# Optimization experiments

Measured on AMD Instinct MI355X. Metric: run time of the kernel, lower is better.

The kernel has to match this reference:

```python
import jax, jax.numpy as jnp
import numpy as np

B, T, C, H = 4, 2048, 1024, 64  # batch, seq, embedding_size, head_size

def setup_inputs() -> dict:
    key = jax.random.key(0)
    k0, k1, k2, k3 = jax.random.split(key, 4)
    scale = 0.02
    return {
        "x":  jax.random.normal(k0, (B, T, C), dtype=jnp.float32),
        "Wq": jax.random.normal(k1, (H, C), dtype=jnp.float32) * scale,
        "Wk": jax.random.normal(k2, (H, C), dtype=jnp.float32) * scale,
        "Wv": jax.random.normal(k3, (H, C), dtype=jnp.float32) * scale,
    }

def reference(x, Wq, Wk, Wv):
    # Linear(bias=False): y = x @ W^T
    q = jnp.einsum('btc,hc->bth', x, Wq)
    k = jnp.einsum('btc,hc->bth', x, Wk)
    v = jnp.einsum('btc,hc->bth', x, Wv)
    # NOTE: original scales by embedding_size C**-0.5, not head_size
    wei = jnp.einsum('bth,bsh->bts', q, k) * (x.shape[-1] ** -0.5)
    t = x.shape[1]
    causal_mask = jnp.tril(jnp.ones((t, t), dtype=bool))  # [T, T]
    wei = jnp.where(causal_mask, wei, -jnp.inf)
    wei = jax.nn.softmax(wei, axis=-1)
    # dropout = 0.0 -> identity (eval mode)
    out = jnp.einsum('bts,bsh->bth', wei, v)
    return out
```

## Files before the change

### kernel.cpp

```cpp
#include <hip/hip_runtime.h>
#include <hip/hip_bf16.h>

typedef unsigned short u16;
typedef __attribute__((ext_vector_type(8))) __bf16 bf16x8;
typedef __attribute__((ext_vector_type(4))) float f32x4;

#define B_ 4
#define T_ 2048
#define C_ 1024
#define H_ 64
#define NSEG 8

__device__ __forceinline__ u16 f2bf(float f) {
    union { __hip_bfloat16 h; u16 u; } cv;
    cv.h = __float2bfloat16(f);
    return cv.u;
}

__device__ __forceinline__ float bf2f(unsigned v) {
    union { unsigned u; float f; } c; c.u = v << 16; return c.f;
}

__device__ __forceinline__ bf16x8 cvt8r(float4 f0, float4 f1) {
    union { u16 h[8]; bf16x8 v; } ua;
    ua.h[0] = f2bf(f0.x); ua.h[1] = f2bf(f0.y);
    ua.h[2] = f2bf(f0.z); ua.h[3] = f2bf(f0.w);
    ua.h[4] = f2bf(f1.x); ua.h[5] = f2bf(f1.y);
    ua.h[6] = f2bf(f1.z); ua.h[7] = f2bf(f1.w);
    return ua.v;
}

__device__ __forceinline__ void gll16(const void* g, void* l) {
    __builtin_amdgcn_global_load_lds(
        (const __attribute__((address_space(1))) void*)g,
        (__attribute__((address_space(3))) void*)l, 16, 0, 0);
}

__global__ __launch_bounds__(256) void wpack(
    const float* __restrict__ wq, const float* __restrict__ wk,
    const float* __restrict__ wv, u16* __restrict__ wP)
{
    int u    = blockIdx.x * 256 + threadIdx.x;
    int ln   = u & 63;
    int frag = u >> 6;
    int ksg  = frag & 31;
    int j16  = frag >> 5;
    int n    = j16 * 16 + (ln & 15);
    int kb   = ksg * 32 + (ln >> 4) * 8;
    const float* src = (n < 64) ? (wq + (size_t)n * C_)
                     : (n < 128) ? (wk + (size_t)(n - 64) * C_)
                                 : (wv + (size_t)(n - 128) * C_);
    float4 f0 = *(const float4*)(src + kb);
    float4 f1 = *(const float4*)(src + kb + 4);
    *(bf16x8*)(wP + (size_t)u * 8) = cvt8r(f0, f1);
}

__global__ __launch_bounds__(512) void qkv(
    const float* __restrict__ x, const u16* __restrict__ wP,
    u16* __restrict__ qP, u16* __restrict__ kP, u16* __restrict__ vP)
{
    __shared__ __align__(16) char smem[32768];

    const int tid = threadIdx.x;
    const int ln  = tid & 63;
    const int w   = tid >> 6;
    const int m0  = blockIdx.x * 32;

    const int lr = ln & 15;
    const int g  = ln >> 4;
    const int ms = w >> 2;
    const int nh = w & 3;

    f32x4 acc[3] = {};

    const int xrow = w * 4 + (ln >> 4);
    const int xc   = (ln & 15) ^ (xrow & 7);

#define STAGE(BUF, KC)                                                     \
    gll16(x + (size_t)(m0 + xrow) * C_ + (KC) * 64 + xc * 4,               \
          smem + (BUF) * 8192 + w * 1024)

    STAGE(0, 0);
    __syncthreads();

    const int ra  = ms * 16 + lr;
    const int rsw = ra & 7;
    const u16* wbase = wP + (size_t)(nh * 3) * 32 * 64 * 8;

    for (int kc = 0; kc < 16; ++kc) {
        const int buf = kc & 1;
        if (kc < 15) STAGE(buf ^ 1, kc + 1);

        const char* rb = smem + buf * 8192;

        bf16x8 a[2];
        #pragma unroll
        for (int ks = 0; ks < 2; ++ks) {
            int c0 = ks * 8 + g * 2;
            float4 fa = *(const float4*)(rb + ra * 256 + ((c0       ^ rsw) << 4));
            float4 fb = *(const float4*)(rb + ra * 256 + (((c0 + 1) ^ rsw) << 4));
            a[ks] = cvt8r(fa, fb);
        }

        #pragma unroll
        for (int j = 0; j < 3; ++j) {
            #pragma unroll
            for (int ks = 0; ks < 2; ++ks) {
                size_t fragofs = ((size_t)(j * 32 + kc * 2 + ks) * 64 + ln) * 8;
                bf16x8 b = *(const bf16x8*)(wbase + fragofs);
                acc[j] = __builtin_amdgcn_mfma_f32_16x16x32_bf16(a[ks], b, acc[j], 0, 0, 0);
            }
        }

        __syncthreads();
    }
#undef STAGE

    float* tile = (float*)smem;
    #pragma unroll
    for (int j = 0; j < 3; ++j)
        #pragma unroll
        for (int i = 0; i < 4; ++i)
            tile[(ms * 16 + g * 4 + i) * 201 + nh * 48 + j * 16 + lr] = acc[j][i];
    __syncthreads();

    for (int uu = tid; uu < 768; uu += 512) {
        const int ln2 = uu & 63;
        const int lr2 = ln2 & 15;
        const int g2  = ln2 >> 4;
        if (uu < 512) {
            const int isK = uu >> 8;
            const int rem = uu & 255;
            const int u   = rem >> 7;
            const int ks  = (rem >> 6) & 1;
            const float* src = tile + (u * 16 + lr2) * 201 + isK * 64 + ks * 32 + g2 * 8;
            float4 f0 = *(const float4*)src;
            float4 f1 = *(const float4*)(src + 4);
            bf16x8 val = cvt8r(f0, f1);
            u16* dst = (isK ? kP : qP)
                     + ((size_t)(((m0 >> 4) + u) * 2 + ks) * 64 + ln2) * 8;
            *(bf16x8*)dst = val;
        } else {
            const int rem = uu - 512;
            const int jf  = rem >> 6;
            union { u16 h[8]; bf16x8 v; } ua;
            #pragma unroll
            for (int e = 0; e < 8; ++e)
                ua.h[e] = f2bf(tile[(g2 * 8 + e) * 201 + 128 + jf * 16 + lr2]);
            u16* dst = vP + ((size_t)((m0 >> 5) * 4 + jf) * 64 + ln2) * 8;
            *(bf16x8*)dst = ua.v;
        }
    }
}

__global__ __launch_bounds__(64) void attn_part(
    const u16* __restrict__ qP, const u16* __restrict__ kP,
    const u16* __restrict__ vP, u16* __restrict__ opart,
    float* __restrict__ ml)
{
    __shared__ u16 ps[16 * 72];

    const int lane = threadIdx.x;
    const int bid  = blockIdx.x;
    const int seg  = bid & (NSEG - 1);
    const int tix  = bid >> 3;
    const int b    = tix & 3;
    const int qt   = 127 - (tix >> 2);
    const int q0   = qt * 16;

    const int lr = lane & 15;
    const int g  = lane >> 4;
    const int lk = g * 8;

    const int nch = (qt >> 2) + 1;
    const int L   = (nch + NSEG - 1) >> 3;
    const int c0  = seg * L;
    const int c1  = min(nch, c0 + L);

    if (c0 >= c1) {
        if (lr == 0)
            #pragma unroll
            for (int i = 0; i < 4; ++i) {
                ml[(size_t)bid * 32 + (g * 4 + i) * 2]     = -1e30f;
                ml[(size_t)bid * 32 + (g * 4 + i) * 2 + 1] = 0.f;
            }
        return;
    }

    bf16x8 aq[2];
    #pragma unroll
    for (int ks = 0; ks < 2; ++ks)
        aq[ks] = *(const bf16x8*)(qP + ((size_t)((b * 128 + qt) * 2 + ks) * 64 + lane) * 8);

    f32x4 oacc[4] = {};
    float mrow[4], lrow[4];
    #pragma unroll
    for (int i = 0; i < 4; ++i) { mrow[i] = -1e30f; lrow[i] = 0.f; }

    for (int jc = c0; jc < c1; ++jc) {
        const int kv0 = jc << 6;

        bf16x8 bk[8];
        #pragma unroll
        for (int jf = 0; jf < 4; ++jf)
            #pragma unroll
            for (int ks = 0; ks < 2; ++ks)
                bk[jf * 2 + ks] = *(const bf16x8*)(kP +
                    ((size_t)((b * 128 + (kv0 >> 4) + jf) * 2 + ks) * 64 + lane) * 8);

        f32x4 sacc[4] = {};
        #pragma unroll
        for (int jf = 0; jf < 4; ++jf)
            #pragma unroll
            for (int ks = 0; ks < 2; ++ks)
                sacc[jf] = __builtin_amdgcn_mfma_f32_16x16x32_bf16(aq[ks], bk[jf * 2 + ks], sacc[jf], 0, 0, 0);

        bf16x8 bv[8];
        #pragma unroll
        for (int ks2 = 0; ks2 < 2; ++ks2)
            #pragma unroll
            for (int jf = 0; jf < 4; ++jf)
                bv[jf * 2 + ks2] = *(const bf16x8*)(vP +
                    ((size_t)((b * 64 + (kv0 >> 5) + ks2) * 4 + jf) * 64 + lane) * 8);

        const bool full = (kv0 + 63 <= q0);
        #pragma unroll
        for (int jf = 0; jf < 4; ++jf) {
            int col = kv0 + jf * 16 + lr;
            #pragma unroll
            for (int i = 0; i < 4; ++i) {
                int row = q0 + g * 4 + i;
                float val = sacc[jf][i] * 0.03125f;
                sacc[jf][i] = (full || col <= row) ? val : -1e30f;
            }
        }

        float pnew[4][4];
        #pragma unroll
        for (int i = 0; i < 4; ++i) {
            float mx = fmaxf(fmaxf(sacc[0][i], sacc[1][i]), fmaxf(sacc[2][i], sacc[3][i]));
            mx = fmaxf(mx, __shfl_xor(mx, 1));
            mx = fmaxf(mx, __shfl_xor(mx, 2));
            mx = fmaxf(mx, __shfl_xor(mx, 4));
            mx = fmaxf(mx, __shfl_xor(mx, 8));
            float mnew = fmaxf(mrow[i], mx);
            float corr = __expf(mrow[i] - mnew);
            float rs = 0.f;
            #pragma unroll
            for (int jf = 0; jf < 4; ++jf) {
                float p = __expf(sacc[jf][i] - mnew);
                pnew[jf][i] = p;
                rs += p;
            }
            rs += __shfl_xor(rs, 1);
            rs += __shfl_xor(rs, 2);
            rs += __shfl_xor(rs, 4);
            rs += __shfl_xor(rs, 8);
            lrow[i] = lrow[i] * corr + rs;
            mrow[i] = mnew;
            #pragma unroll
            for (int jf = 0; jf < 4; ++jf) oacc[jf][i] *= corr;
        }

        #pragma unroll
        for (int jf = 0; jf < 4; ++jf)
            #pragma unroll
            for (int i = 0; i < 4; ++i)
                ps[(g * 4 + i) * 72 + jf * 16 + lr] = f2bf(pnew[jf][i]);

        #pragma unroll
        for (int ks2 = 0; ks2 < 2; ++ks2) {
            bf16x8 ap = *(const bf16x8*)(ps + lr * 72 + ks2 * 32 + lk);
            #pragma unroll
            for (int jf = 0; jf < 4; ++jf)
                oacc[jf] = __builtin_amdgcn_mfma_f32_16x16x32_bf16(ap, bv[jf * 2 + ks2], oacc[jf], 0, 0, 0);
        }
    }

    #pragma unroll
    for (int jf = 0; jf < 4; ++jf)
        #pragma unroll
        for (int i = 0; i < 4; ++i)
            opart[(size_t)bid * 1024 + (g * 4 + i) * 64 + jf * 16 + lr] = f2bf(oacc[jf][i]);
    if (lr == 0)
        #pragma unroll
        for (int i = 0; i < 4; ++i) {
            ml[(size_t)bid * 32 + (g * 4 + i) * 2]     = mrow[i];
            ml[(size_t)bid * 32 + (g * 4 + i) * 2 + 1] = lrow[i];
        }
}

__global__ __launch_bounds__(256) void attn_reduce(
    const u16* __restrict__ opart, const float* __restrict__ ml,
    float* __restrict__ out)
{
    const int t   = blockIdx.x;
    const int row = threadIdx.x >> 4;
    const int p   = threadIdx.x & 15;
    const int b   = t & 3;
    const int qt  = 127 - (t >> 2);

    float m[NSEG], l[NSEG];
    #pragma unroll
    for (int s = 0; s < NSEG; ++s) {
        m[s] = ml[(size_t)(t * NSEG + s) * 32 + row * 2];
        l[s] = ml[(size_t)(t * NSEG + s) * 32 + row * 2 + 1];
    }
    float M = m[0];
    #pragma unroll
    for (int s = 1; s < NSEG; ++s) M = fmaxf(M, m[s]);

    float a0 = 0.f, a1 = 0.f, a2 = 0.f, a3 = 0.f, Lsum = 0.f;
    #pragma unroll
    for (int s = 0; s < NSEG; ++s) {
        float wgt = __expf(m[s] - M);
        Lsum += l[s] * wgt;
        uint2 o = *(const uint2*)(opart + (size_t)(t * NSEG + s) * 1024 + row * 64 + p * 4);
        a0 += wgt * bf2f(o.x & 0xffffu);
        a1 += wgt * bf2f(o.x >> 16);
        a2 += wgt * bf2f(o.y & 0xffffu);
        a3 += wgt * bf2f(o.y >> 16);
    }
    float inv = 1.f / Lsum;
    float4 r; r.x = a0 * inv; r.y = a1 * inv; r.z = a2 * inv; r.w = a3 * inv;
    *(float4*)(out + ((size_t)b * T_ + qt * 16 + row) * H_ + p * 4) = r;
}

extern "C" void kernel_launch(void* const* d_in, const int* in_sizes, int n_in,
                              void* d_out, int out_size, void* d_ws, size_t ws_size,
                              hipStream_t stream) {
    const float* x  = (const float*)d_in[0];
    const float* wq = (const float*)d_in[1];
    const float* wk = (const float*)d_in[2];
    const float* wv = (const float*)d_in[3];

    u16* qPws = (u16*)d_ws;
    u16* kPws = qPws + (size_t)B_ * T_ * H_;
    u16* vPws = kPws + (size_t)B_ * T_ * H_;
    u16* wPws = vPws + (size_t)B_ * T_ * H_;
    u16* opart = wPws + (size_t)192 * C_;
    float* mlbuf = (float*)(opart + (size_t)4096 * 1024);

    wpack<<<96, 256, 0, stream>>>(wq, wk, wv, wPws);
    qkv<<<256, 512, 0, stream>>>(x, wPws, qPws, kPws, vPws);
    attn_part<<<4096, 64, 0, stream>>>(qPws, kPws, vPws, opart, mlbuf);
    attn_reduce<<<512, 256, 0, stream>>>(opart, mlbuf, (float*)d_out);
}
```

Measured before the change: 41.14 us.

## Pack four attention units per block, add MFMA priority and mask-only-last-chunk

Groups four independent single-wave work units into one 256-thread block with per-wave LDS scratch, cutting block count and launch/scheduling overhead. Adds s_setprio around MFMA sections so matrix work is favoured among co-resident waves. The causal mask is applied only on the final diagonal chunk instead of a per-element check every iteration. The reduce kernel also skips segments with zero row sum, avoiding loads for empty partitions. Packing waves that finish at different times into one block may leave block slots held longer.

```diff
diff --git a/kernel.cpp b/kernel.cpp
--- a/kernel.cpp
+++ b/kernel.cpp
@@ -153,17 +153,18 @@
     }
 }
 
-__global__ __launch_bounds__(64) void attn_part(
+__global__ __launch_bounds__(256) void attn_part(
     const u16* __restrict__ qP, const u16* __restrict__ kP,
     const u16* __restrict__ vP, u16* __restrict__ opart,
     float* __restrict__ ml)
 {
-    __shared__ u16 ps[16 * 72];
-
-    const int lane = threadIdx.x;
-    const int bid  = blockIdx.x;
-    const int seg  = bid & (NSEG - 1);
-    const int tix  = bid >> 3;
+    __shared__ u16 ps[4][16 * 72];
+
+    const int lane = threadIdx.x & 63;
+    const int w    = threadIdx.x >> 6;
+    const int unit = blockIdx.x * 4 + w;
+    const int seg  = unit & (NSEG - 1);
+    const int tix  = unit >> 3;
     const int b    = tix & 3;
     const int qt   = 127 - (tix >> 2);
     const int q0   = qt * 16;
@@ -181,11 +182,13 @@
         if (lr == 0)
             #pragma unroll
             for (int i = 0; i < 4; ++i) {
-                ml[(size_t)bid * 32 + (g * 4 + i) * 2]     = -1e30f;
-                ml[(size_t)bid * 32 + (g * 4 + i) * 2 + 1] = 0.f;
+                ml[(size_t)unit * 32 + (g * 4 + i) * 2]     = -1e30f;
+                ml[(size_t)unit * 32 + (g * 4 + i) * 2 + 1] = 0.f;
             }
         return;
     }
+
+    u16* myps = ps[w];
 
     bf16x8 aq[2];
     #pragma unroll
@@ -209,11 +212,13 @@
                     ((size_t)((b * 128 + (kv0 >> 4) + jf) * 2 + ks) * 64 + lane) * 8);
 
         f32x4 sacc[4] = {};
+        __builtin_amdgcn_s_setprio(1);
         #pragma unroll
         for (int jf = 0; jf < 4; ++jf)
             #pragma unroll
             for (int ks = 0; ks < 2; ++ks)
                 sacc[jf] = __builtin_amdgcn_mfma_f32_16x16x32_bf16(aq[ks], bk[jf * 2 + ks], sacc[jf], 0, 0, 0);
+        __builtin_amdgcn_s_setprio(0);
 
         bf16x8 bv[8];
         #pragma unroll
@@ -223,15 +228,22 @@
                 bv[jf * 2 + ks2] = *(const bf16x8*)(vP +
                     ((size_t)((b * 64 + (kv0 >> 5) + ks2) * 4 + jf) * 64 + lane) * 8);
 
-        const bool full = (kv0 + 63 <= q0);
-        #pragma unroll
-        for (int jf = 0; jf < 4; ++jf) {
-            int col = kv0 + jf * 16 + lr;
-            #pragma unroll
-            for (int i = 0; i < 4; ++i) {
-                int row = q0 + g * 4 + i;
-                float val = sacc[jf][i] * 0.03125f;
-                sacc[jf][i] = (full || col <= row) ? val : -1e30f;
+        if (jc != nch - 1) {
+            #pragma unroll
+            for (int jf = 0; jf < 4; ++jf)
+                #pragma unroll
+                for (int i = 0; i < 4; ++i)
+                    sacc[jf][i] *= 0.03125f;
+        } else {
+            #pragma unroll
+            for (int jf = 0; jf < 4; ++jf) {
+                int col = kv0 + jf * 16 + lr;
+                #pragma unroll
+                for (int i = 0; i < 4; ++i) {
+                    int row = q0 + g * 4 + i;
+                    float val = sacc[jf][i] * 0.03125f;
+                    sacc[jf][i] = (col <= row) ? val : -1e30f;
+                }
             }
         }
 
@@ -266,27 +278,29 @@
         for (int jf = 0; jf < 4; ++jf)
             #pragma unroll
             for (int i = 0; i < 4; ++i)
-                ps[(g * 4 + i) * 72 + jf * 16 + lr] = f2bf(pnew[jf][i]);
-
+                myps[(g * 4 + i) * 72 + jf * 16 + lr] = f2bf(pnew[jf][i]);
+
+        __builtin_amdgcn_s_setprio(1);
         #pragma unroll
         for (int ks2 = 0; ks2 < 2; ++ks2) {
-            bf16x8 ap = *(const bf16x8*)(ps + lr * 72 + ks2 * 32 + lk);
+            bf16x8 ap = *(const bf16x8*)(myps + lr * 72 + ks2 * 32 + lk);
             #pragma unroll
             for (int jf = 0; jf < 4; ++jf)
                 oacc[jf] = __builtin_amdgcn_mfma_f32_16x16x32_bf16(ap, bv[jf * 2 + ks2], oacc[jf], 0, 0, 0);
         }
+        __builtin_amdgcn_s_setprio(0);
     }
 
     #pragma unroll
     for (int jf = 0; jf < 4; ++jf)
         #pragma unroll
         for (int i = 0; i < 4; ++i)
-            opart[(size_t)bid * 1024 + (g * 4 + i) * 64 + jf * 16 + lr] = f2bf(oacc[jf][i]);
+            opart[(size_t)unit * 1024 + (g * 4 + i) * 64 + jf * 16 + lr] = f2bf(oacc[jf][i]);
     if (lr == 0)
         #pragma unroll
         for (int i = 0; i < 4; ++i) {
-            ml[(size_t)bid * 32 + (g * 4 + i) * 2]     = mrow[i];
-            ml[(size_t)bid * 32 + (g * 4 + i) * 2 + 1] = lrow[i];
+            ml[(size_t)unit * 32 + (g * 4 + i) * 2]     = mrow[i];
+            ml[(size_t)unit * 32 + (g * 4 + i) * 2 + 1] = lrow[i];
         }
 }
 
@@ -313,13 +327,15 @@
     float a0 = 0.f, a1 = 0.f, a2 = 0.f, a3 = 0.f, Lsum = 0.f;
     #pragma unroll
     for (int s = 0; s < NSEG; ++s) {
-        float wgt = __expf(m[s] - M);
-        Lsum += l[s] * wgt;
-        uint2 o = *(const uint2*)(opart + (size_t)(t * NSEG + s) * 1024 + row * 64 + p * 4);
-        a0 += wgt * bf2f(o.x & 0xffffu);
-        a1 += wgt * bf2f(o.x >> 16);
-        a2 += wgt * bf2f(o.y & 0xffffu);
-        a3 += wgt * bf2f(o.y >> 16);
+        if (l[s] != 0.f) {
+            float wgt = __expf(m[s] - M);
+            Lsum += l[s] * wgt;
+            uint2 o = *(const uint2*)(opart + (size_t)(t * NSEG + s) * 1024 + row * 64 + p * 4);
+            a0 += wgt * bf2f(o.x & 0xffffu);
+            a1 += wgt * bf2f(o.x >> 16);
+            a2 += wgt * bf2f(o.y & 0xffffu);
+            a3 += wgt * bf2f(o.y >> 16);
+        }
     }
     float inv = 1.f / Lsum;
     float4 r; r.x = a0 * inv; r.y = a1 * inv; r.z = a2 * inv; r.w = a3 * inv;
@@ -343,6 +359,6 @@
 
     wpack<<<96, 256, 0, stream>>>(wq, wk, wv, wPws);
     qkv<<<256, 512, 0, stream>>>(x, wPws, qPws, kPws, vPws);
-    attn_part<<<4096, 64, 0, stream>>>(qPws, kPws, vPws, opart, mlbuf);
+    attn_part<<<1024, 256, 0, stream>>>(qPws, kPws, vPws, opart, mlbuf);
     attn_reduce<<<512, 256, 0, stream>>>(opart, mlbuf, (float*)d_out);
 }
```

New measurement: 44.74 us. +8.7%, slower.
